# Performance work log

Hardware: AMD Instinct MI355X
Metric: run time of the kernel (lower is better)

## Reference

```python
import jax, jax.numpy as jnp
import numpy as np

B_SZ, L, D, N = 64, 100, 16, 1024

def setup_inputs() -> dict:
    key = jax.random.key(0)
    ks = jax.random.split(key, 8)
    s = 1.0 / np.sqrt(D)  # ~ torch Linear init scale
    x  = jax.random.normal(ks[0], (B_SZ, L, D), dtype=jnp.float32)
    W1 = jax.random.normal(ks[1], (D, D), dtype=jnp.float32) * s
    b1 = jnp.zeros((D,), dtype=jnp.float32)
    W2 = jax.random.normal(ks[2], (D, N), dtype=jnp.float32) * s
    b2 = jnp.zeros((N,), dtype=jnp.float32)
    W3 = jax.random.normal(ks[3], (D, N), dtype=jnp.float32) * s
    b3 = jnp.zeros((N,), dtype=jnp.float32)
    # A = repeat(arange(1, N+1), 'n -> d n'); A_log = log(A)
    A_log = jnp.log(jnp.broadcast_to(jnp.arange(1, N + 1, dtype=jnp.float32), (D, N)))
    return {"x": x, "W1": W1, "b1": b1, "W2": W2, "b2": b2, "W3": W3, "b3": b3, "A_log": A_log}


def reference(x, W1, b1, W2, b2, W3, b3, A_log):
    # Projections (torch Linear with weights stored as [in, out])
    delta = jax.nn.softplus(x @ W1 + b1)          # (b, l, d)
    Bm = x @ W2 + b2                              # (b, l, n)
    Cm = x @ W3 + b3                              # (b, l, n)
    # Discretization
    A = -jnp.exp(A_log)                           # (d, n)
    dA = jnp.exp(jnp.einsum('bld,dn->bldn', delta, A))   # (b, l, d, n)
    dB = jnp.einsum('bld,bln->bldn', delta, Bm)           # (b, l, d, n)
    # h initialized to zeros in the source forward, so dA * h == 0
    h = dA * 0.0 + x[..., None] * dB              # (b, l, d, n)
    y = jnp.einsum('bln,bldn->bld', Cm, h)        # (b, l, d)
    return y
```

## Files before the change

### kernel.cpp

```cpp
#include <hip/hip_runtime.h>
#include <math.h>


#define DD 16
#define NN 1024

__global__ __launch_bounds__(256) void s6_precompute(
    const float* __restrict__ W2, const float* __restrict__ b2,
    const float* __restrict__ W3, const float* __restrict__ b3,
    float* __restrict__ ws)
{
    int wave = blockIdx.x * 4 + (threadIdx.x >> 6);
    int lane = threadIdx.x & 63;
    float acc = 0.f;
    if (wave < 256) {
        int i = wave >> 4, j = wave & 15;
        const float* r2 = W2 + i * NN;
        const float* r3 = W3 + j * NN;
        #pragma unroll
        for (int w = 0; w < 4; ++w) {
            int n0 = w * 256 + lane * 4;
            float4 a = *(const float4*)(r2 + n0);
            float4 b = *(const float4*)(r3 + n0);
            acc += a.x*b.x + a.y*b.y + a.z*b.z + a.w*b.w;
        }
    } else if (wave < 272) {
        int i = wave - 256;
        const float* r2 = W2 + i * NN;
        const float* r3 = W3 + i * NN;
        #pragma unroll
        for (int w = 0; w < 4; ++w) {
            int n0 = w * 256 + lane * 4;
            float4 a2 = *(const float4*)(r2 + n0);
            float4 a3 = *(const float4*)(r3 + n0);
            float4 v2 = *(const float4*)(b2 + n0);
            float4 v3 = *(const float4*)(b3 + n0);
            acc += a2.x*v3.x + a2.y*v3.y + a2.z*v3.z + a2.w*v3.w;
            acc += a3.x*v2.x + a3.y*v2.y + a3.z*v2.z + a3.w*v2.w;
        }
    } else if (wave == 272) {
        #pragma unroll
        for (int w = 0; w < 4; ++w) {
            int n0 = w * 256 + lane * 4;
            float4 v2 = *(const float4*)(b2 + n0);
            float4 v3 = *(const float4*)(b3 + n0);
            acc += v2.x*v3.x + v2.y*v3.y + v2.z*v3.z + v2.w*v3.w;
        }
    } else {
        return;
    }
    #pragma unroll
    for (int o = 32; o >= 1; o >>= 1) acc += __shfl_xor(acc, o, 64);
    if (lane == 0) ws[wave] = acc;
}

__global__ __launch_bounds__(256) void s6_fused(
    const float* __restrict__ x, const float* __restrict__ W1,
    const float* __restrict__ b1, const float* __restrict__ ws,
    float* __restrict__ out)
{
    __shared__ float xs[256];
    __shared__ float w1s[256];
    __shared__ float b1s[DD];
    __shared__ float uvs[DD];
    __shared__ float ms[DD * 17];

    const int tid  = threadIdx.x;
    const int base = blockIdx.x * 256;

    xs[tid]  = x[base + tid];
    w1s[tid] = W1[tid];
    ms[(tid >> 4) * 17 + (tid & 15)] = ws[tid];
    if (tid < DD) { b1s[tid] = b1[tid]; uvs[tid] = ws[256 + tid]; }
    const float c = ws[272];
    __syncthreads();

    const int g = tid >> 4, d = tid & 15;

    float v[DD];
    #pragma unroll
    for (int k = 0; k < DD; ++k) v[k] = xs[g * DD + k];

    float td = b1s[d];
    #pragma unroll
    for (int k = 0; k < DD; ++k) td = fmaf(v[k], w1s[k * DD + d], td);
    const float delta = fmaxf(td, 0.f) + log1pf(expf(-fabsf(td)));

    float row = uvs[d];
    #pragma unroll
    for (int j = 0; j < DD; ++j) row = fmaf(ms[d * 17 + j], v[j], row);
    float p = v[d] * row;
    #pragma unroll
    for (int o = 1; o < 16; o <<= 1) p += __shfl_xor(p, o, 64);
    const float s = p + c;

    out[base + tid] = v[d] * delta * s;
}

extern "C" void kernel_launch(void* const* d_in, const int* in_sizes, int n_in,
                              void* d_out, int out_size, void* d_ws, size_t ws_size,
                              hipStream_t stream) {
    const float* x  = (const float*)d_in[0];
    const float* W1 = (const float*)d_in[1];
    const float* b1 = (const float*)d_in[2];
    const float* W2 = (const float*)d_in[3];
    const float* b2 = (const float*)d_in[4];
    const float* W3 = (const float*)d_in[5];
    const float* b3 = (const float*)d_in[6];
    float* out = (float*)d_out;
    float* ws  = (float*)d_ws;

    s6_precompute<<<69, 256, 0, stream>>>(W2, b2, W3, b3, ws);
    s6_fused<<<400, 256, 0, stream>>>(x, W1, b1, ws, out);
}
```

Baseline: 12.46 us.

## Fuse precompute into single kernel with per-block bf16 MFMA Gram matrix

Merges the two launches into one kernel where every block recomputes the 16x16 W2·W3ᵀ Gram matrix using bf16 MFMA, plus the bias cross terms, then processes 64 tokens per block across 100 blocks. This removes the second kernel launch and the global workspace round trip, at the cost of redundant weight reads and compute in every block. Converting the weights to bf16 reduces the precision of the Gram matrix relative to the fp32 reference.

```diff
diff --git a/kernel.cpp b/kernel.cpp
--- a/kernel.cpp
+++ b/kernel.cpp
@@ -4,97 +4,122 @@
 
 #define DD 16
 #define NN 1024
+#define TOKS 64
+#define NBLK 100
 
-__global__ __launch_bounds__(256) void s6_precompute(
+typedef __attribute__((ext_vector_type(8))) short bf16x8;
+typedef __attribute__((ext_vector_type(4))) float f32x4;
+
+static __device__ inline short f2bf(float f) {
+    union { float f; unsigned u; } v; v.f = f;
+    unsigned r = v.u + 0x7FFFu + ((v.u >> 16) & 1u);
+    return (short)(r >> 16);
+}
+
+__global__ __launch_bounds__(256) void s6_all(
+    const float* __restrict__ x,  const float* __restrict__ W1,
+    const float* __restrict__ b1,
     const float* __restrict__ W2, const float* __restrict__ b2,
     const float* __restrict__ W3, const float* __restrict__ b3,
-    float* __restrict__ ws)
-{
-    int wave = blockIdx.x * 4 + (threadIdx.x >> 6);
-    int lane = threadIdx.x & 63;
-    float acc = 0.f;
-    if (wave < 256) {
-        int i = wave >> 4, j = wave & 15;
-        const float* r2 = W2 + i * NN;
-        const float* r3 = W3 + j * NN;
-        #pragma unroll
-        for (int w = 0; w < 4; ++w) {
-            int n0 = w * 256 + lane * 4;
-            float4 a = *(const float4*)(r2 + n0);
-            float4 b = *(const float4*)(r3 + n0);
-            acc += a.x*b.x + a.y*b.y + a.z*b.z + a.w*b.w;
-        }
-    } else if (wave < 272) {
-        int i = wave - 256;
-        const float* r2 = W2 + i * NN;
-        const float* r3 = W3 + i * NN;
-        #pragma unroll
-        for (int w = 0; w < 4; ++w) {
-            int n0 = w * 256 + lane * 4;
-            float4 a2 = *(const float4*)(r2 + n0);
-            float4 a3 = *(const float4*)(r3 + n0);
-            float4 v2 = *(const float4*)(b2 + n0);
-            float4 v3 = *(const float4*)(b3 + n0);
-            acc += a2.x*v3.x + a2.y*v3.y + a2.z*v3.z + a2.w*v3.w;
-            acc += a3.x*v2.x + a3.y*v2.y + a3.z*v2.z + a3.w*v2.w;
-        }
-    } else if (wave == 272) {
-        #pragma unroll
-        for (int w = 0; w < 4; ++w) {
-            int n0 = w * 256 + lane * 4;
-            float4 v2 = *(const float4*)(b2 + n0);
-            float4 v3 = *(const float4*)(b3 + n0);
-            acc += v2.x*v3.x + v2.y*v3.y + v2.z*v3.z + v2.w*v3.w;
-        }
-    } else {
-        return;
-    }
-    #pragma unroll
-    for (int o = 32; o >= 1; o >>= 1) acc += __shfl_xor(acc, o, 64);
-    if (lane == 0) ws[wave] = acc;
-}
-
-__global__ __launch_bounds__(256) void s6_fused(
-    const float* __restrict__ x, const float* __restrict__ W1,
-    const float* __restrict__ b1, const float* __restrict__ ws,
     float* __restrict__ out)
 {
-    __shared__ float xs[256];
+    __shared__ float xs[TOKS * DD];
     __shared__ float w1s[256];
     __shared__ float b1s[DD];
+    __shared__ float part[4][256];
+    __shared__ float ms[DD * 17];
     __shared__ float uvs[DD];
-    __shared__ float ms[DD * 17];
+    __shared__ float cs;
 
     const int tid  = threadIdx.x;
-    const int base = blockIdx.x * 256;
+    const int wv   = tid >> 6;
+    const int lane = tid & 63;
+    const int base = blockIdx.x * (TOKS * DD);
 
-    xs[tid]  = x[base + tid];
+    *(float4*)(xs + tid * 4) = *(const float4*)(x + base + tid * 4);
     w1s[tid] = W1[tid];
-    ms[(tid >> 4) * 17 + (tid & 15)] = ws[tid];
-    if (tid < DD) { b1s[tid] = b1[tid]; uvs[tid] = ws[256 + tid]; }
-    const float c = ws[272];
+    if (tid < DD) b1s[tid] = b1[tid];
+
+    {
+        const int r  = lane & 15;
+        const int kg = lane >> 4;
+        const float* a_base = W2 + r * NN + wv * 256 + kg * 8;
+        const float* b_base = W3 + r * NN + wv * 256 + kg * 8;
+        f32x4 acc = {0.f, 0.f, 0.f, 0.f};
+        #pragma unroll
+        for (int kk = 0; kk < 8; ++kk) {
+            float4 a0 = *(const float4*)(a_base + kk * 32);
+            float4 a1 = *(const float4*)(a_base + kk * 32 + 4);
+            float4 c0 = *(const float4*)(b_base + kk * 32);
+            float4 c1 = *(const float4*)(b_base + kk * 32 + 4);
+            bf16x8 af, bf;
+            af[0]=f2bf(a0.x); af[1]=f2bf(a0.y); af[2]=f2bf(a0.z); af[3]=f2bf(a0.w);
+            af[4]=f2bf(a1.x); af[5]=f2bf(a1.y); af[6]=f2bf(a1.z); af[7]=f2bf(a1.w);
+            bf[0]=f2bf(c0.x); bf[1]=f2bf(c0.y); bf[2]=f2bf(c0.z); bf[3]=f2bf(c0.w);
+            bf[4]=f2bf(c1.x); bf[5]=f2bf(c1.y); bf[6]=f2bf(c1.z); bf[7]=f2bf(c1.w);
+            acc = __builtin_amdgcn_mfma_f32_16x16x32_bf16(af, bf, acc, 0, 0, 0);
+        }
+        #pragma unroll
+        for (int ri = 0; ri < 4; ++ri)
+            part[wv][((lane >> 4) * 4 + ri) * 16 + (lane & 15)] = acc[ri];
+    }
+
+    {
+        const int i = tid >> 4, d = tid & 15;
+        const float* r2 = W2 + i * NN + d * 64;
+        const float* r3 = W3 + i * NN + d * 64;
+        const float* p2 = b2 + d * 64;
+        const float* p3 = b3 + d * 64;
+        float uvp = 0.f, cp = 0.f;
+        #pragma unroll
+        for (int t = 0; t < 16; ++t) {
+            float4 a2 = *(const float4*)(r2 + t * 4);
+            float4 a3 = *(const float4*)(r3 + t * 4);
+            float4 v2 = *(const float4*)(p2 + t * 4);
+            float4 v3 = *(const float4*)(p3 + t * 4);
+            uvp += a2.x*v3.x + a2.y*v3.y + a2.z*v3.z + a2.w*v3.w
+                 + a3.x*v2.x + a3.y*v2.y + a3.z*v2.z + a3.w*v2.w;
+            cp  += v2.x*v3.x + v2.y*v3.y + v2.z*v3.z + v2.w*v3.w;
+        }
+        #pragma unroll
+        for (int o = 1; o < 16; o <<= 1) {
+            uvp += __shfl_xor(uvp, o, 64);
+            cp  += __shfl_xor(cp,  o, 64);
+        }
+        if (d == 0) uvs[i] = uvp;
+        if (tid == 0) cs = cp;
+    }
+
+    __syncthreads();
+
+    ms[(tid >> 4) * 17 + (tid & 15)] =
+        part[0][tid] + part[1][tid] + part[2][tid] + part[3][tid];
+
     __syncthreads();
 
     const int g = tid >> 4, d = tid & 15;
+    const float c = cs;
+    #pragma unroll
+    for (int tt = 0; tt < TOKS / 16; ++tt) {
+        const float* vv = xs + (tt * 16 + g) * DD;
+        float v[DD];
+        #pragma unroll
+        for (int k = 0; k < DD; ++k) v[k] = vv[k];
 
-    float v[DD];
-    #pragma unroll
-    for (int k = 0; k < DD; ++k) v[k] = xs[g * DD + k];
+        float td = b1s[d];
+        #pragma unroll
+        for (int k = 0; k < DD; ++k) td = fmaf(v[k], w1s[k * DD + d], td);
+        const float delta = fmaxf(td, 0.f) + log1pf(expf(-fabsf(td)));
 
-    float td = b1s[d];
-    #pragma unroll
-    for (int k = 0; k < DD; ++k) td = fmaf(v[k], w1s[k * DD + d], td);
-    const float delta = fmaxf(td, 0.f) + log1pf(expf(-fabsf(td)));
+        float row = uvs[d];
+        #pragma unroll
+        for (int j = 0; j < DD; ++j) row = fmaf(ms[d * 17 + j], v[j], row);
+        float p = v[d] * row;
+        #pragma unroll
+        for (int o = 1; o < 16; o <<= 1) p += __shfl_xor(p, o, 64);
 
-    float row = uvs[d];
-    #pragma unroll
-    for (int j = 0; j < DD; ++j) row = fmaf(ms[d * 17 + j], v[j], row);
-    float p = v[d] * row;
-    #pragma unroll
-    for (int o = 1; o < 16; o <<= 1) p += __shfl_xor(p, o, 64);
-    const float s = p + c;
-
-    out[base + tid] = v[d] * delta * s;
+        out[base + tt * 256 + tid] = v[d] * delta * (p + c);
+    }
 }
 
 extern "C" void kernel_launch(void* const* d_in, const int* in_sizes, int n_in,
@@ -108,8 +133,6 @@
     const float* W3 = (const float*)d_in[5];
     const float* b3 = (const float*)d_in[6];
     float* out = (float*)d_out;
-    float* ws  = (float*)d_ws;
 
-    s6_precompute<<<69, 256, 0, stream>>>(W2, b2, W3, b3, ws);
-    s6_fused<<<400, 256, 0, stream>>>(x, W1, b1, ws, out);
+    s6_all<<<NBLK, 256, 0, stream>>>(x, W1, b1, W2, b2, W3, b3, out);
 }
```

Measured after the change: 19.71 us. 58.2% more time.
